# Kernel optimization log

Hardware: AMD Instinct MI355X
Metric: run time of the kernel (lower is better)

Reference implementation:

```python
import jax, jax.numpy as jnp
import numpy as np

B, S, D, P = 16, 128, 768, 1024
N_CLASSES = 121  # dataset != 'restaurant'


def setup_inputs() -> dict:
    key = jax.random.key(0)
    ks = jax.random.split(key, 8)
    scale = lambda fan_in: 1.0 / np.sqrt(fan_in)
    return {
        "spans_embedding": jax.random.normal(ks[0], (B, S, D), dtype=jnp.float32),
        "W1": jax.random.normal(ks[1], (3 * D, 2 * D), dtype=jnp.float32) * scale(3 * D),
        "b1": jnp.zeros((2 * D,), dtype=jnp.float32),
        "W2": jax.random.normal(ks[2], (2 * D, D), dtype=jnp.float32) * scale(2 * D),
        "b2": jnp.zeros((D,), dtype=jnp.float32),
        "W3": jax.random.normal(ks[3], (D, N_CLASSES), dtype=jnp.float32) * scale(D),
        "b3": jnp.zeros((N_CLASSES,), dtype=jnp.float32),
        "span_masks": jnp.ones((B, S), dtype=jnp.int32),
        "batch_idx": jax.random.randint(ks[4], (P,), 0, B, dtype=jnp.int64),
        "aspect_idx": jax.random.randint(ks[5], (P,), 0, S - 2, dtype=jnp.int64),
        "opinion_idx": jax.random.randint(ks[6], (P,), 0, S - 2, dtype=jnp.int64),
    }


def reference(spans_embedding, W1, b1, W2, b2, W3, b3,
              span_masks, batch_idx, aspect_idx, opinion_idx):
    S_ = spans_embedding.shape[1]
    pos = jnp.arange(S_)
    last = jnp.sum(span_masks, axis=1) - 1          # [B] last valid span index
    li = last[batch_idx]                             # [P]
    emb = spans_embedding[batch_idx]                 # [P, S, D] gathered per pair

    def rng_max(lo, hi):                             # max over spans in [lo, hi)
        mask = (pos[None, :] >= lo[:, None]) & (pos[None, :] < hi[:, None])
        return jnp.max(jnp.where(mask[:, :, None], emb, -jnp.inf), axis=1)

    def rng_mean(lo, hi):                            # mean over spans in [lo, hi)
        m = ((pos[None, :] >= lo[:, None]) & (pos[None, :] < hi[:, None])).astype(emb.dtype)
        cnt = jnp.maximum(jnp.sum(m, axis=1), 1.0)
        return jnp.einsum('ps,psd->pd', m, emb) / cnt[:, None]

    ones = jnp.ones_like(aspect_idx)
    # boundary index b: aspect when aspect!=0, else opinion (matches all non-both-zero branches)
    b = jnp.where(aspect_idx != 0, aspect_idx, opinion_idx)
    emb0 = spans_embedding[batch_idx, 0]             # [P, D]
    embL = spans_embedding[batch_idx, li]            # [P, D]
    left_nz = jnp.where((b == 1)[:, None], emb0, rng_max(ones, b))
    right_nz = jnp.where((b == li)[:, None], embL, rng_max(b, li))

    both0 = (aspect_idx == 0) & (opinion_idx == 0)
    left = jnp.where(both0[:, None], rng_mean(ones, li), left_nz)
    right = jnp.where(both0[:, None], rng_max(ones, li), right_nz)

    aspect_rep = spans_embedding[batch_idx, aspect_idx]
    o_eff = jnp.where(opinion_idx == 0, li, opinion_idx)
    opinion_rep = spans_embedding[batch_idx, o_eff]

    x = jnp.concatenate([aspect_rep + opinion_rep, left, right], axis=1)  # [P, 3D]
    h = jax.nn.relu(x @ W1 + b1)
    h = jax.nn.relu(h @ W2 + b2)
    return h @ W3 + b3                               # [P, n_classes]
```

## Files before the change

### kernel.cpp

```cpp
#include <hip/hip_runtime.h>
#include <hip/hip_bf16.h>
#include <math.h>

#define S_LEN 128
#define D_DIM 768
#define P_PAIRS 1024
#define B_BATCH 16

typedef __attribute__((ext_vector_type(8))) short bf16x8;
typedef __attribute__((ext_vector_type(4))) float f32x4;

#define PB_UNITS (B_BATCH * (D_DIM / 64))
#define T1_UNITS ((2304 / 64) * (1536 / 64))
#define T2_UNITS ((1536 / 64) * (768 / 64))
#define T3_UNITS ((768 / 64) * (128 / 64))

union SmemU {
    struct {
        ushort semb[128][64];
        ushort spref[128][64];
        ushort ssuf[128][64];
        ushort smean[64];
        float  lred[3][4][64];
        int    li;
    } pb;
    float t64[64][65];
};

__device__ __forceinline__ ushort f2bf(float f) {
    __hip_bfloat16 h = __float2bfloat16(f);
    return *(ushort*)&h;
}

__device__ __forceinline__ float bf2f(ushort u) {
    unsigned int x = ((unsigned int)u) << 16;
    float f;
    __builtin_memcpy(&f, &x, 4);
    return f;
}

__device__ __forceinline__ void gload16(const void* g, void* l) {
    __builtin_amdgcn_global_load_lds(
        (const __attribute__((address_space(1))) void*)g,
        (__attribute__((address_space(3))) void*)l, 16, 0, 0);
}

__global__ __launch_bounds__(256) void fused_prep_kernel(
    const float* __restrict__ emb_all,
    const int* __restrict__ span_masks,
    const int* __restrict__ batch_idx,
    const int* __restrict__ aspect_idx,
    const int* __restrict__ opinion_idx,
    ushort* __restrict__ X,
    const float* __restrict__ W1, ushort* __restrict__ W1t,
    const float* __restrict__ W2, ushort* __restrict__ W2t,
    const float* __restrict__ W3, ushort* __restrict__ W3t)
{
    __shared__ SmemU sm;
    int bid = blockIdx.x;
    int tid = threadIdx.x;

    if (bid < PB_UNITS) {
        int b = bid / (D_DIM / 64);
        int chunk = bid % (D_DIM / 64);
        int lane = tid & 63;
        int g = tid >> 6;
        int r0 = g * 32;
        int col = chunk * 64 + lane;

        if (tid == 0) {
            int s = 0;
            for (int i = 0; i < S_LEN; ++i) s += span_masks[b * S_LEN + i];
            sm.pb.li = s - 1;
        }
        __syncthreads();
        int li = sm.pb.li;

        const float* embb = emb_all + (size_t)b * S_LEN * D_DIM;

        float v[32];
        #pragma unroll
        for (int r = 0; r < 32; ++r) {
            v[r] = embb[(size_t)(r0 + r) * D_DIM + col];
            sm.pb.semb[r0 + r][lane] = f2bf(v[r]);
        }

        float wmax = -INFINITY, umax = -INFINITY, s = 0.f;
        #pragma unroll
        for (int r = 0; r < 32; ++r) {
            int gr = r0 + r;
            wmax = fmaxf(wmax, (gr == 0) ? -INFINITY : v[r]);
            bool in = (gr >= 1) && (gr < li);
            umax = fmaxf(umax, in ? v[r] : -INFINITY);
            s += in ? v[r] : 0.f;
        }
        sm.pb.lred[0][g][lane] = wmax;
        sm.pb.lred[1][g][lane] = umax;
        sm.pb.lred[2][g][lane] = s;
        __syncthreads();

        float basep = -INFINITY;
        #pragma unroll
        for (int gg = 0; gg < 3; ++gg)
            if (gg < g) basep = fmaxf(basep, sm.pb.lred[0][gg][lane]);
        float bases = -INFINITY;
        #pragma unroll
        for (int gg = 1; gg < 4; ++gg)
            if (gg > g) bases = fmaxf(bases, sm.pb.lred[1][gg][lane]);

        if (g == 0) {
            float tot = sm.pb.lred[2][0][lane] + sm.pb.lred[2][1][lane]
                      + sm.pb.lred[2][2][lane] + sm.pb.lred[2][3][lane];
            int cnt = (li - 1) > 0 ? (li - 1) : 1;
            sm.pb.smean[lane] = f2bf(tot / (float)cnt);
        }

        float m = basep;
        #pragma unroll
        for (int r = 0; r < 32; ++r) {
            int gr = r0 + r;
            m = fmaxf(m, (gr == 0) ? -INFINITY : v[r]);
            sm.pb.spref[gr][lane] = f2bf(m);
        }
        float m2 = bases;
        #pragma unroll
        for (int r = 31; r >= 0; --r) {
            int gr = r0 + r;
            bool in = (gr >= 1) && (gr < li);
            m2 = fmaxf(m2, in ? v[r] : -INFINITY);
            if (gr >= 1) sm.pb.ssuf[gr][lane] = f2bf(m2);
        }
        __syncthreads();

        int pbase = g * 256;
        for (int c = 0; c < 256; c += 64) {
            int p = pbase + c + lane;
            int vb = batch_idx[p];
            int va = aspect_idx[p];
            int vo = opinion_idx[p];
            unsigned long long mask = __ballot(vb == b);
            while (mask) {
                int i = __ffsll((long long)mask) - 1;
                mask &= mask - 1;
                int pp = pbase + c + i;
                int a = __shfl(va, i);
                int o = __shfl(vo, i);
                bool both0 = (a == 0) && (o == 0);
                int bnd = (a != 0) ? a : o;
                int oe = (o == 0) ? li : o;
                float ar  = bf2f(sm.pb.semb[a][lane]);
                float orp = bf2f(sm.pb.semb[oe][lane]);
                ushort left, right;
                if (both0) {
                    left  = sm.pb.smean[lane];
                    right = sm.pb.spref[li - 1][lane];
                } else {
                    left  = (bnd == 1)  ? sm.pb.semb[0][lane]
                                        : sm.pb.spref[bnd - 1][lane];
                    right = (bnd == li) ? sm.pb.semb[li][lane]
                                        : sm.pb.ssuf[bnd][lane];
                }
                size_t base = (size_t)pp * (3 * D_DIM) + col;
                X[base]             = f2bf(ar + orp);
                X[base + D_DIM]     = left;
                X[base + 2 * D_DIM] = right;
            }
        }
    } else {
        int tb = bid - PB_UNITS;
        const float* in; ushort* out; int K, N, Npad, bx, by;
        if (tb < T1_UNITS) {
            in = W1; out = W1t; K = 2304; N = 1536; Npad = 1536;
            bx = tb % (2304 / 64); by = tb / (2304 / 64);
        } else if (tb < T1_UNITS + T2_UNITS) {
            tb -= T1_UNITS;
            in = W2; out = W2t; K = 1536; N = 768; Npad = 768;
            bx = tb % (1536 / 64); by = tb / (1536 / 64);
        } else {
            tb -= T1_UNITS + T2_UNITS;
            in = W3; out = W3t; K = 768; N = 121; Npad = 128;
            bx = tb % (768 / 64); by = tb / (768 / 64);
        }
        int k0 = bx * 64, n0 = by * 64;

        int kr = tid >> 2;
        int nq = (tid & 3) * 16;
        if (n0 + 64 <= N) {
            #pragma unroll
            for (int j = 0; j < 4; ++j) {
                float4 vv = *(const float4*)&in[(size_t)(k0 + kr) * N + n0 + nq + j * 4];
                *(float4*)&sm.t64[kr][nq + j * 4] = vv;
            }
        } else {
            #pragma unroll
            for (int j = 0; j < 16; ++j) {
                int n = n0 + nq + j;
                sm.t64[kr][nq + j] = (n < N) ? in[(size_t)(k0 + kr) * N + n] : 0.f;
            }
        }
        __syncthreads();

        int nr = tid >> 2;
        int kq = (tid & 3) * 16;
        if (n0 + nr < Npad) {
            ushort tmp[16];
            #pragma unroll
            for (int j = 0; j < 16; ++j) tmp[j] = f2bf(sm.t64[kq + j][nr]);
            ushort* dst = out + (size_t)(n0 + nr) * K + k0 + kq;
            *(bf16x8*)dst       = *(bf16x8*)&tmp[0];
            *(bf16x8*)(dst + 8) = *(bf16x8*)&tmp[8];
        }
    }
}

template<int WRITE_BF16, int RELU>
__global__ __launch_bounds__(256) void gemm_mfma96(
    const ushort* __restrict__ A,
    const ushort* __restrict__ Bt,
    const float* __restrict__ bias,
    void* __restrict__ Cout,
    int M, int N, int K)
{
    __shared__ ushort lds[3][160 * 64];
    int tid = threadIdx.x;
    int lane = tid & 63;
    int w = tid >> 6;
    int wr = w >> 1, wc = w & 1;
    int rl = lane & 15;

    int id = blockIdx.y * 16 + blockIdx.x;
    int swz = (id & 7) * 32 + (id >> 3);
    int bx = swz % 16;
    int by = swz / 16;

    int rowBase = by * 64;
    int colBase = bx * 96;

    int srow  = lane >> 3;
    int scolb = (((lane & 7) ^ srow) << 4);
    const char* Abase = (const char*)(A  + (size_t)rowBase * K);
    const char* Bbase = (const char*)(Bt + (size_t)colBase * K);
    size_t rstride = (size_t)K * 2;
    const char* Badj = Bbase - (size_t)64 * rstride;

    f32x4 acc[2][3] = {};
    int nt = K >> 6;

    auto stage = [&](int buf, int t) {
        size_t kb0 = (size_t)t << 7;
        #pragma unroll
        for (int i = 0; i < 5; ++i) {
            int g = w * 5 + i;
            const char* eb = (g < 8) ? Abase : Badj;
            gload16(eb + (size_t)(g * 8 + srow) * rstride + kb0 + scolb,
                    &lds[buf][g * 512]);
        }
    };

    stage(0, 0);
    stage(1, 1);

    int cur = 0;
    for (int t = 0; t < nt; ++t) {
        if (t + 1 < nt) asm volatile("s_waitcnt vmcnt(5)" ::: "memory");
        else            asm volatile("s_waitcnt vmcnt(0)" ::: "memory");
        __builtin_amdgcn_s_barrier();
        __builtin_amdgcn_sched_barrier(0);

        if (t + 2 < nt) stage((t + 2) % 3, t + 2);

        const char* lb = (const char*)&lds[cur][0];
        int kq = (lane >> 4) << 4;
        bf16x8 af[2][2], bfr[3][2];
        #pragma unroll
        for (int m = 0; m < 2; ++m) {
            int row = wr * 32 + m * 16 + rl;
            #pragma unroll
            for (int kk = 0; kk < 2; ++kk) {
                int addr = row * 128 + ((kq + kk * 64) ^ ((row & 7) << 4));
                af[m][kk] = *(const bf16x8*)(lb + addr);
            }
        }
        #pragma unroll
        for (int n = 0; n < 3; ++n) {
            int row = 64 + wc * 48 + n * 16 + rl;
            #pragma unroll
            for (int kk = 0; kk < 2; ++kk) {
                int addr = row * 128 + ((kq + kk * 64) ^ ((row & 7) << 4));
                bfr[n][kk] = *(const bf16x8*)(lb + addr);
            }
        }
        __builtin_amdgcn_s_setprio(1);
        #pragma unroll
        for (int m = 0; m < 2; ++m)
            #pragma unroll
            for (int n = 0; n < 3; ++n)
                #pragma unroll
                for (int kk = 0; kk < 2; ++kk)
                    acc[m][n] = __builtin_amdgcn_mfma_f32_16x16x32_bf16(
                        af[m][kk], bfr[n][kk], acc[m][n], 0, 0, 0);
        __builtin_amdgcn_s_setprio(0);
        cur = (cur + 1) % 3;
    }

    #pragma unroll
    for (int m = 0; m < 2; ++m) {
        #pragma unroll
        for (int n = 0; n < 3; ++n) {
            #pragma unroll
            for (int j = 0; j < 4; ++j) {
                int row = rowBase + wr * 32 + m * 16 + (lane >> 4) * 4 + j;
                int col = colBase + wc * 48 + n * 16 + rl;
                if (col < N && row < M) {
                    float v = acc[m][n][j] + bias[col];
                    if (RELU) v = fmaxf(v, 0.f);
                    if (WRITE_BF16)
                        ((ushort*)Cout)[(size_t)row * N + col] = f2bf(v);
                    else
                        ((float*)Cout)[(size_t)row * N + col] = v;
                }
            }
        }
    }
}

template<int WRITE_BF16, int RELU>
__global__ __launch_bounds__(256, 3) void gemm_mfma(
    const ushort* __restrict__ A,
    const ushort* __restrict__ Bt,
    const float* __restrict__ bias,
    void* __restrict__ Cout,
    int M, int N, int K)
{
    __shared__ ushort lds[3][128 * 64];
    int tid = threadIdx.x;
    int lane = tid & 63;
    int w = tid >> 6;
    int wr = w >> 1, wc = w & 1;

    int gx = gridDim.x;
    int id = blockIdx.y * gx + blockIdx.x;
    int n8 = (gx * gridDim.y) >> 3;
    int swz = (id & 7) * n8 + (id >> 3);
    int bx = swz % gx;
    int by = swz / gx;

    int rowBase = by * 64;
    int colBase = bx * 64;

    int srow  = lane >> 3;
    int scolb = (((lane & 7) ^ srow) << 4);
    const char* Abase = (const char*)(A  + (size_t)rowBase * K);
    const char* Bbase = (const char*)(Bt + (size_t)colBase * K);
    size_t rstride = (size_t)K * 2;

    f32x4 acc[2][2] = {};
    int nt = K >> 6;

    auto stage = [&](int buf, int t) {
        size_t kb0 = (size_t)t << 7;
        #pragma unroll
        for (int i = 0; i < 2; ++i) {
            int r = w * 16 + i * 8 + srow;
            gload16(Abase + (size_t)r * rstride + kb0 + scolb,
                    &lds[buf][(w * 16 + i * 8) * 64]);
        }
        #pragma unroll
        for (int i = 0; i < 2; ++i) {
            int r = w * 16 + i * 8 + srow;
            gload16(Bbase + (size_t)r * rstride + kb0 + scolb,
                    &lds[buf][(64 + w * 16 + i * 8) * 64]);
        }
    };

    stage(0, 0);
    stage(1, 1);

    int cur = 0;
    for (int t = 0; t < nt; ++t) {
        if (t + 1 < nt) asm volatile("s_waitcnt vmcnt(4)" ::: "memory");
        else            asm volatile("s_waitcnt vmcnt(0)" ::: "memory");
        __builtin_amdgcn_s_barrier();
        __builtin_amdgcn_sched_barrier(0);

        if (t + 2 < nt) stage((t + 2) % 3, t + 2);

        const char* lb = (const char*)&lds[cur][0];
        int kq = (lane >> 4) << 4;
        bf16x8 af[2][2], bfr[2][2];
        #pragma unroll
        for (int m = 0; m < 2; ++m) {
            int row = wr * 32 + m * 16 + (lane & 15);
            #pragma unroll
            for (int kk = 0; kk < 2; ++kk) {
                int addr = row * 128 + ((kq + kk * 64) ^ ((row & 7) << 4));
                af[m][kk] = *(const bf16x8*)(lb + addr);
            }
        }
        #pragma unroll
        for (int n = 0; n < 2; ++n) {
            int row = 64 + wc * 32 + n * 16 + (lane & 15);
            #pragma unroll
            for (int kk = 0; kk < 2; ++kk) {
                int addr = row * 128 + ((kq + kk * 64) ^ ((row & 7) << 4));
                bfr[n][kk] = *(const bf16x8*)(lb + addr);
            }
        }
        __builtin_amdgcn_s_setprio(1);
        #pragma unroll
        for (int m = 0; m < 2; ++m)
            #pragma unroll
            for (int n = 0; n < 2; ++n)
                #pragma unroll
                for (int kk = 0; kk < 2; ++kk)
                    acc[m][n] = __builtin_amdgcn_mfma_f32_16x16x32_bf16(
                        af[m][kk], bfr[n][kk], acc[m][n], 0, 0, 0);
        __builtin_amdgcn_s_setprio(0);
        cur = (cur + 1) % 3;
    }

    #pragma unroll
    for (int m = 0; m < 2; ++m) {
        #pragma unroll
        for (int n = 0; n < 2; ++n) {
            #pragma unroll
            for (int j = 0; j < 4; ++j) {
                int row = rowBase + wr * 32 + m * 16 + (lane >> 4) * 4 + j;
                int col = colBase + wc * 32 + n * 16 + (lane & 15);
                if (col < N && row < M) {
                    float v = acc[m][n][j] + bias[col];
                    if (RELU) v = fmaxf(v, 0.f);
                    if (WRITE_BF16)
                        ((ushort*)Cout)[(size_t)row * N + col] = f2bf(v);
                    else
                        ((float*)Cout)[(size_t)row * N + col] = v;
                }
            }
        }
    }
}

extern "C" void kernel_launch(void* const* d_in, const int* in_sizes, int n_in,
                              void* d_out, int out_size, void* d_ws, size_t ws_size,
                              hipStream_t stream) {
    const float* emb        = (const float*)d_in[0];
    const float* W1         = (const float*)d_in[1];
    const float* b1         = (const float*)d_in[2];
    const float* W2         = (const float*)d_in[3];
    const float* b2         = (const float*)d_in[4];
    const float* W3         = (const float*)d_in[5];
    const float* b3         = (const float*)d_in[6];
    const int* span_masks   = (const int*)d_in[7];
    const int* batch_idx    = (const int*)d_in[8];
    const int* aspect_idx   = (const int*)d_in[9];
    const int* opinion_idx  = (const int*)d_in[10];
    float* out = (float*)d_out;

    ushort* Xb  = (ushort*)d_ws;
    ushort* H2  = Xb;
    ushort* W1t = Xb  + (size_t)1024 * 2304;
    ushort* W2t = W1t + (size_t)1536 * 2304;
    ushort* W3t = W2t + (size_t)768 * 1536;
    ushort* H1  = W3t + (size_t)128 * 768;

    fused_prep_kernel<<<PB_UNITS + T1_UNITS + T2_UNITS + T3_UNITS, 256, 0, stream>>>(
        emb, span_masks, batch_idx, aspect_idx, opinion_idx, Xb,
        W1, W1t, W2, W2t, W3, W3t);

    gemm_mfma96<1,1><<<dim3(1536/96, 1024/64), 256, 0, stream>>>(Xb, W1t, b1, H1, 1024, 1536, 2304);
    gemm_mfma  <1,1><<<dim3( 768/64, 1024/64), 256, 0, stream>>>(H1, W2t, b2, H2, 1024, 768, 1536);
    gemm_mfma  <0,0><<<dim3( 128/64, 1024/64), 256, 0, stream>>>(H2, W3t, b3, out, 1024, 121, 768);
}
```

Baseline: 56.06 us.

## Fuse second and third GEMMs with atomic split-K output, widen transpose tiles

The second and third MLP layers now run in one kernel. Each 64x64 tile of the second layer's output is kept in LDS, multiplied by the matching slice of W3, and the partial logits are accumulated into the output with atomicAdd. The prep kernel gains extra blocks that zero the output first, and its weight-transpose blocks now each handle 128 K-rows. The first GEMM goes back to the generic 64x64 kernel in place of the 96-wide variant. This removes one launch and the H2 round trip through memory, at the cost of 12-way float atomic contention on the output and nondeterministic summation order.

```diff
diff --git a/kernel.cpp b/kernel.cpp
--- a/kernel.cpp
+++ b/kernel.cpp
@@ -11,9 +11,12 @@
 typedef __attribute__((ext_vector_type(4))) float f32x4;
 
 #define PB_UNITS (B_BATCH * (D_DIM / 64))
-#define T1_UNITS ((2304 / 64) * (1536 / 64))
-#define T2_UNITS ((1536 / 64) * (768 / 64))
-#define T3_UNITS ((768 / 64) * (128 / 64))
+#define T1_UNITS ((2304 / 128) * (1536 / 64))
+#define T2_UNITS ((1536 / 128) * (768 / 64))
+#define T3_UNITS ((768 / 128) * (128 / 64))
+#define ZERO_BASE (PB_UNITS + T1_UNITS + T2_UNITS + T3_UNITS)
+#define ZERO_BLOCKS 8
+#define PREP_BLOCKS (ZERO_BASE + ZERO_BLOCKS)
 
 union SmemU {
     struct {
@@ -24,7 +27,7 @@
         float  lred[3][4][64];
         int    li;
     } pb;
-    float t64[64][65];
+    float t128[128][65];
 };
 
 __device__ __forceinline__ ushort f2bf(float f) {
@@ -54,7 +57,8 @@
     ushort* __restrict__ X,
     const float* __restrict__ W1, ushort* __restrict__ W1t,
     const float* __restrict__ W2, ushort* __restrict__ W2t,
-    const float* __restrict__ W3, ushort* __restrict__ W3t)
+    const float* __restrict__ W3, ushort* __restrict__ W3t,
+    float* __restrict__ outp)
 {
     __shared__ SmemU sm;
     int bid = blockIdx.x;
@@ -166,170 +170,70 @@
                 X[base + 2 * D_DIM] = right;
             }
         }
-    } else {
+    } else if (bid < ZERO_BASE) {
         int tb = bid - PB_UNITS;
         const float* in; ushort* out; int K, N, Npad, bx, by;
         if (tb < T1_UNITS) {
             in = W1; out = W1t; K = 2304; N = 1536; Npad = 1536;
-            bx = tb % (2304 / 64); by = tb / (2304 / 64);
+            bx = tb % (2304 / 128); by = tb / (2304 / 128);
         } else if (tb < T1_UNITS + T2_UNITS) {
             tb -= T1_UNITS;
             in = W2; out = W2t; K = 1536; N = 768; Npad = 768;
-            bx = tb % (1536 / 64); by = tb / (1536 / 64);
+            bx = tb % (1536 / 128); by = tb / (1536 / 128);
         } else {
             tb -= T1_UNITS + T2_UNITS;
             in = W3; out = W3t; K = 768; N = 121; Npad = 128;
-            bx = tb % (768 / 64); by = tb / (768 / 64);
-        }
-        int k0 = bx * 64, n0 = by * 64;
-
-        int kr = tid >> 2;
-        int nq = (tid & 3) * 16;
-        if (n0 + 64 <= N) {
-            #pragma unroll
-            for (int j = 0; j < 4; ++j) {
-                float4 vv = *(const float4*)&in[(size_t)(k0 + kr) * N + n0 + nq + j * 4];
-                *(float4*)&sm.t64[kr][nq + j * 4] = vv;
-            }
-        } else {
-            #pragma unroll
-            for (int j = 0; j < 16; ++j) {
-                int n = n0 + nq + j;
-                sm.t64[kr][nq + j] = (n < N) ? in[(size_t)(k0 + kr) * N + n] : 0.f;
+            bx = tb % (768 / 128); by = tb / (768 / 128);
+        }
+        int k0 = bx * 128, n0 = by * 64;
+
+        #pragma unroll
+        for (int h = 0; h < 2; ++h) {
+            int kr = h * 64 + (tid >> 2);
+            int nq = (tid & 3) * 16;
+            if (n0 + 64 <= N) {
+                #pragma unroll
+                for (int j = 0; j < 4; ++j) {
+                    float4 vv = *(const float4*)&in[(size_t)(k0 + kr) * N + n0 + nq + j * 4];
+                    *(float4*)&sm.t128[kr][nq + j * 4] = vv;
+                }
+            } else {
+                #pragma unroll
+                for (int j = 0; j < 16; ++j) {
+                    int n = n0 + nq + j;
+                    sm.t128[kr][nq + j] = (n < N) ? in[(size_t)(k0 + kr) * N + n] : 0.f;
+                }
             }
         }
         __syncthreads();
 
         int nr = tid >> 2;
-        int kq = (tid & 3) * 16;
+        int kq = (tid & 3) * 32;
         if (n0 + nr < Npad) {
-            ushort tmp[16];
-            #pragma unroll
-            for (int j = 0; j < 16; ++j) tmp[j] = f2bf(sm.t64[kq + j][nr]);
+            ushort tmp[32];
+            #pragma unroll
+            for (int j = 0; j < 32; ++j) tmp[j] = f2bf(sm.t128[kq + j][nr]);
             ushort* dst = out + (size_t)(n0 + nr) * K + k0 + kq;
-            *(bf16x8*)dst       = *(bf16x8*)&tmp[0];
-            *(bf16x8*)(dst + 8) = *(bf16x8*)&tmp[8];
-        }
-    }
-}
-
-template<int WRITE_BF16, int RELU>
-__global__ __launch_bounds__(256) void gemm_mfma96(
-    const ushort* __restrict__ A,
-    const ushort* __restrict__ Bt,
-    const float* __restrict__ bias,
-    void* __restrict__ Cout,
-    int M, int N, int K)
-{
-    __shared__ ushort lds[3][160 * 64];
-    int tid = threadIdx.x;
-    int lane = tid & 63;
-    int w = tid >> 6;
-    int wr = w >> 1, wc = w & 1;
-    int rl = lane & 15;
-
-    int id = blockIdx.y * 16 + blockIdx.x;
-    int swz = (id & 7) * 32 + (id >> 3);
-    int bx = swz % 16;
-    int by = swz / 16;
-
-    int rowBase = by * 64;
-    int colBase = bx * 96;
-
-    int srow  = lane >> 3;
-    int scolb = (((lane & 7) ^ srow) << 4);
-    const char* Abase = (const char*)(A  + (size_t)rowBase * K);
-    const char* Bbase = (const char*)(Bt + (size_t)colBase * K);
-    size_t rstride = (size_t)K * 2;
-    const char* Badj = Bbase - (size_t)64 * rstride;
-
-    f32x4 acc[2][3] = {};
-    int nt = K >> 6;
-
-    auto stage = [&](int buf, int t) {
-        size_t kb0 = (size_t)t << 7;
-        #pragma unroll
-        for (int i = 0; i < 5; ++i) {
-            int g = w * 5 + i;
-            const char* eb = (g < 8) ? Abase : Badj;
-            gload16(eb + (size_t)(g * 8 + srow) * rstride + kb0 + scolb,
-                    &lds[buf][g * 512]);
-        }
-    };
-
-    stage(0, 0);
-    stage(1, 1);
-
-    int cur = 0;
-    for (int t = 0; t < nt; ++t) {
-        if (t + 1 < nt) asm volatile("s_waitcnt vmcnt(5)" ::: "memory");
-        else            asm volatile("s_waitcnt vmcnt(0)" ::: "memory");
-        __builtin_amdgcn_s_barrier();
-        __builtin_amdgcn_sched_barrier(0);
-
-        if (t + 2 < nt) stage((t + 2) % 3, t + 2);
-
-        const char* lb = (const char*)&lds[cur][0];
-        int kq = (lane >> 4) << 4;
-        bf16x8 af[2][2], bfr[3][2];
-        #pragma unroll
-        for (int m = 0; m < 2; ++m) {
-            int row = wr * 32 + m * 16 + rl;
-            #pragma unroll
-            for (int kk = 0; kk < 2; ++kk) {
-                int addr = row * 128 + ((kq + kk * 64) ^ ((row & 7) << 4));
-                af[m][kk] = *(const bf16x8*)(lb + addr);
-            }
-        }
-        #pragma unroll
-        for (int n = 0; n < 3; ++n) {
-            int row = 64 + wc * 48 + n * 16 + rl;
-            #pragma unroll
-            for (int kk = 0; kk < 2; ++kk) {
-                int addr = row * 128 + ((kq + kk * 64) ^ ((row & 7) << 4));
-                bfr[n][kk] = *(const bf16x8*)(lb + addr);
-            }
-        }
-        __builtin_amdgcn_s_setprio(1);
-        #pragma unroll
-        for (int m = 0; m < 2; ++m)
-            #pragma unroll
-            for (int n = 0; n < 3; ++n)
-                #pragma unroll
-                for (int kk = 0; kk < 2; ++kk)
-                    acc[m][n] = __builtin_amdgcn_mfma_f32_16x16x32_bf16(
-                        af[m][kk], bfr[n][kk], acc[m][n], 0, 0, 0);
-        __builtin_amdgcn_s_setprio(0);
-        cur = (cur + 1) % 3;
-    }
-
-    #pragma unroll
-    for (int m = 0; m < 2; ++m) {
-        #pragma unroll
-        for (int n = 0; n < 3; ++n) {
-            #pragma unroll
-            for (int j = 0; j < 4; ++j) {
-                int row = rowBase + wr * 32 + m * 16 + (lane >> 4) * 4 + j;
-                int col = colBase + wc * 48 + n * 16 + rl;
-                if (col < N && row < M) {
-                    float v = acc[m][n][j] + bias[col];
-                    if (RELU) v = fmaxf(v, 0.f);
-                    if (WRITE_BF16)
-                        ((ushort*)Cout)[(size_t)row * N + col] = f2bf(v);
-                    else
-                        ((float*)Cout)[(size_t)row * N + col] = v;
-                }
-            }
-        }
-    }
-}
-
-template<int WRITE_BF16, int RELU>
+            *(bf16x8*)(dst)      = *(bf16x8*)&tmp[0];
+            *(bf16x8*)(dst + 8)  = *(bf16x8*)&tmp[8];
+            *(bf16x8*)(dst + 16) = *(bf16x8*)&tmp[16];
+            *(bf16x8*)(dst + 24) = *(bf16x8*)&tmp[24];
+        }
+    } else {
+        int zb = bid - ZERO_BASE;
+        float4 z = {0.f, 0.f, 0.f, 0.f};
+        int idx = zb * 256 + tid;
+        const int total4 = (P_PAIRS * 121) / 4;
+        for (int i = idx; i < total4; i += ZERO_BLOCKS * 256)
+            ((float4*)outp)[i] = z;
+    }
+}
+
 __global__ __launch_bounds__(256, 3) void gemm_mfma(
     const ushort* __restrict__ A,
     const ushort* __restrict__ Bt,
     const float* __restrict__ bias,
-    void* __restrict__ Cout,
+    ushort* __restrict__ Cout,
     int M, int N, int K)
 {
     __shared__ ushort lds[3][128 * 64];
@@ -427,14 +331,153 @@
             for (int j = 0; j < 4; ++j) {
                 int row = rowBase + wr * 32 + m * 16 + (lane >> 4) * 4 + j;
                 int col = colBase + wc * 32 + n * 16 + (lane & 15);
-                if (col < N && row < M) {
-                    float v = acc[m][n][j] + bias[col];
-                    if (RELU) v = fmaxf(v, 0.f);
-                    if (WRITE_BF16)
-                        ((ushort*)Cout)[(size_t)row * N + col] = f2bf(v);
-                    else
-                        ((float*)Cout)[(size_t)row * N + col] = v;
-                }
+                float v = fmaxf(acc[m][n][j] + bias[col], 0.f);
+                Cout[(size_t)row * N + col] = f2bf(v);
+            }
+        }
+    }
+}
+
+__global__ __launch_bounds__(256, 2) void gemm23_fused(
+    const ushort* __restrict__ A,
+    const ushort* __restrict__ Bt,
+    const float* __restrict__ bias2,
+    const ushort* __restrict__ W3t,
+    const float* __restrict__ bias3,
+    float* __restrict__ outp)
+{
+    constexpr int K = 1536, N = 768, NOUT = 121;
+    __shared__ ushort lds[3][128 * 64];
+    int tid = threadIdx.x;
+    int lane = tid & 63;
+    int w = tid >> 6;
+    int wr = w >> 1, wc = w & 1;
+
+    int id = blockIdx.y * 12 + blockIdx.x;
+    int swz = (id & 7) * 24 + (id >> 3);
+    int bx = swz % 12;
+    int by = swz / 12;
+
+    int rowBase = by * 64;
+    int colBase = bx * 64;
+
+    int srow  = lane >> 3;
+    int scolb = (((lane & 7) ^ srow) << 4);
+    const char* Abase = (const char*)(A  + (size_t)rowBase * K);
+    const char* Bbase = (const char*)(Bt + (size_t)colBase * K);
+    size_t rstride = (size_t)K * 2;
+
+    f32x4 acc[2][2] = {};
+    int nt = K >> 6;
+
+    auto stage = [&](int buf, int t) {
+        size_t kb0 = (size_t)t << 7;
+        #pragma unroll
+        for (int i = 0; i < 2; ++i) {
+            int r = w * 16 + i * 8 + srow;
+            gload16(Abase + (size_t)r * rstride + kb0 + scolb,
+                    &lds[buf][(w * 16 + i * 8) * 64]);
+        }
+        #pragma unroll
+        for (int i = 0; i < 2; ++i) {
+            int r = w * 16 + i * 8 + srow;
+            gload16(Bbase + (size_t)r * rstride + kb0 + scolb,
+                    &lds[buf][(64 + w * 16 + i * 8) * 64]);
+        }
+    };
+
+    stage(0, 0);
+    stage(1, 1);
+
+    int cur = 0;
+    for (int t = 0; t < nt; ++t) {
+        if (t + 1 < nt) asm volatile("s_waitcnt vmcnt(4)" ::: "memory");
+        else            asm volatile("s_waitcnt vmcnt(0)" ::: "memory");
+        __builtin_amdgcn_s_barrier();
+        __builtin_amdgcn_sched_barrier(0);
+
+        if (t + 2 < nt) stage((t + 2) % 3, t + 2);
+
+        const char* lb = (const char*)&lds[cur][0];
+        int kq = (lane >> 4) << 4;
+        bf16x8 af[2][2], bfr[2][2];
+        #pragma unroll
+        for (int m = 0; m < 2; ++m) {
+            int row = wr * 32 + m * 16 + (lane & 15);
+            #pragma unroll
+            for (int kk = 0; kk < 2; ++kk) {
+                int addr = row * 128 + ((kq + kk * 64) ^ ((row & 7) << 4));
+                af[m][kk] = *(const bf16x8*)(lb + addr);
+            }
+        }
+        #pragma unroll
+        for (int n = 0; n < 2; ++n) {
+            int row = 64 + wc * 32 + n * 16 + (lane & 15);
+            #pragma unroll
+            for (int kk = 0; kk < 2; ++kk) {
+                int addr = row * 128 + ((kq + kk * 64) ^ ((row & 7) << 4));
+                bfr[n][kk] = *(const bf16x8*)(lb + addr);
+            }
+        }
+        __builtin_amdgcn_s_setprio(1);
+        #pragma unroll
+        for (int m = 0; m < 2; ++m)
+            #pragma unroll
+            for (int n = 0; n < 2; ++n)
+                #pragma unroll
+                for (int kk = 0; kk < 2; ++kk)
+                    acc[m][n] = __builtin_amdgcn_mfma_f32_16x16x32_bf16(
+                        af[m][kk], bfr[n][kk], acc[m][n], 0, 0, 0);
+        __builtin_amdgcn_s_setprio(0);
+        cur = (cur + 1) % 3;
+    }
+
+    __syncthreads();
+    char* hb = (char*)&lds[0][0];
+    #pragma unroll
+    for (int m = 0; m < 2; ++m) {
+        #pragma unroll
+        for (int n = 0; n < 2; ++n) {
+            #pragma unroll
+            for (int j = 0; j < 4; ++j) {
+                int row = wr * 32 + m * 16 + (lane >> 4) * 4 + j;
+                int col = wc * 32 + n * 16 + (lane & 15);
+                float v = fmaxf(acc[m][n][j] + bias2[colBase + col], 0.f);
+                int byte = row * 128 + ((col * 2) ^ ((row & 7) << 4));
+                *(ushort*)(hb + byte) = f2bf(v);
+            }
+        }
+    }
+    __syncthreads();
+
+    f32x4 acc2[8] = {};
+    #pragma unroll
+    for (int kk = 0; kk < 2; ++kk) {
+        int ar = w * 16 + (lane & 15);
+        int kb = kk * 64 + ((lane >> 4) << 4);
+        bf16x8 af = *(const bf16x8*)(hb + ar * 128 + (kb ^ ((ar & 7) << 4)));
+        bf16x8 b3f[8];
+        #pragma unroll
+        for (int n = 0; n < 8; ++n) {
+            int r3 = n * 16 + (lane & 15);
+            int k3 = colBase + kk * 32 + (lane >> 4) * 8;
+            b3f[n] = *(const bf16x8*)(W3t + (size_t)r3 * N + k3);
+        }
+        #pragma unroll
+        for (int n = 0; n < 8; ++n)
+            acc2[n] = __builtin_amdgcn_mfma_f32_16x16x32_bf16(af, b3f[n], acc2[n], 0, 0, 0);
+    }
+
+    bool addb = (bx == 0);
+    #pragma unroll
+    for (int n = 0; n < 8; ++n) {
+        #pragma unroll
+        for (int j = 0; j < 4; ++j) {
+            int row = rowBase + w * 16 + (lane >> 4) * 4 + j;
+            int col = n * 16 + (lane & 15);
+            if (col < NOUT) {
+                float v = acc2[n][j] + (addb ? bias3[col] : 0.f);
+                atomicAdd(&outp[(size_t)row * NOUT + col], v);
             }
         }
     }
@@ -457,17 +500,18 @@
     float* out = (float*)d_out;
 
     ushort* Xb  = (ushort*)d_ws;
-    ushort* H2  = Xb;
     ushort* W1t = Xb  + (size_t)1024 * 2304;
     ushort* W2t = W1t + (size_t)1536 * 2304;
     ushort* W3t = W2t + (size_t)768 * 1536;
     ushort* H1  = W3t + (size_t)128 * 768;
 
-    fused_prep_kernel<<<PB_UNITS + T1_UNITS + T2_UNITS + T3_UNITS, 256, 0, stream>>>(
+    fused_prep_kernel<<<PREP_BLOCKS, 256, 0, stream>>>(
         emb, span_masks, batch_idx, aspect_idx, opinion_idx, Xb,
-        W1, W1t, W2, W2t, W3, W3t);
-
-    gemm_mfma96<1,1><<<dim3(1536/96, 1024/64), 256, 0, stream>>>(Xb, W1t, b1, H1, 1024, 1536, 2304);
-    gemm_mfma  <1,1><<<dim3( 768/64, 1024/64), 256, 0, stream>>>(H1, W2t, b2, H2, 1024, 768, 1536);
-    gemm_mfma  <0,0><<<dim3( 128/64, 1024/64), 256, 0, stream>>>(H2, W3t, b3, out, 1024, 121, 768);
-}
+        W1, W1t, W2, W2t, W3, W3t, out);
+
+    gemm_mfma<<<dim3(1536/64, 1024/64), 256, 0, stream>>>(
+        Xb, W1t, b1, H1, 1024, 1536, 2304);
+
+    gemm23_fused<<<dim3(12, 16), 256, 0, stream>>>(
+        H1, W2t, b2, W3t, b3, out);
+}
```

New measurement: 57.85 us. +3.2%, slower.
